# Kernel tuning notes

Measured on AMD Instinct MI355X. Metric: run time of the kernel, lower is better.

Reference implementation:

```python
import jax, jax.numpy as jnp
import numpy as np

N_NODES = 50000
N_EDGES = 800000
F_IN = 256
F_OUT = 64
HEADS = 4
LEAKY_ALPHA = 0.2


def setup_inputs() -> dict:
    key = jax.random.key(0)
    ks = jax.random.split(key, 8)
    x = jax.random.normal(ks[0], (N_NODES, F_IN), dtype=jnp.float32)
    W = jax.random.normal(ks[1], (HEADS, F_IN, F_OUT), dtype=jnp.float32) * 0.05
    a_self = jax.random.normal(ks[2], (HEADS, F_OUT), dtype=jnp.float32) * 0.05
    a_neigh = jax.random.normal(ks[3], (HEADS, F_OUT), dtype=jnp.float32) * 0.05
    bias = jnp.zeros((HEADS, F_OUT), dtype=jnp.float32)
    adj_val = jnp.ones((N_EDGES,), dtype=jnp.float32)
    edge_row = jax.random.randint(ks[4], (N_EDGES,), 0, N_NODES, dtype=jnp.int32)
    edge_col = jax.random.randint(ks[5], (N_EDGES,), 0, N_NODES, dtype=jnp.int32)
    return {"x": x, "W": W, "a_self": a_self, "a_neigh": a_neigh,
            "bias": bias, "adj_val": adj_val,
            "edge_row": edge_row, "edge_col": edge_col}


def reference(x, W, a_self, a_neigh, bias, adj_val, edge_row, edge_col):
    N = x.shape[0]
    # per-head projected features: [H, N, F_out]
    feats = jnp.einsum('nf,hfo->hno', x, W)
    # attention logits per node: [H, N]
    s_self = jnp.einsum('hno,ho->hn', feats, a_self)
    s_neigh = jnp.einsum('hno,ho->hn', feats, a_neigh)
    # edge scores at sparse adjacency positions: [H, E]
    z = s_self[:, edge_row] + s_neigh[:, edge_col]
    e = jnp.where(z > 0, z, LEAKY_ALPHA * z) * adj_val[None, :]

    def seg_softmax(e_h):
        # sparse softmax over each row's nonzero entries
        m = jax.ops.segment_max(e_h, edge_row, num_segments=N)
        ex = jnp.exp(e_h - m[edge_row])
        s = jax.ops.segment_sum(ex, edge_row, num_segments=N)
        return ex / s[edge_row]

    alpha = jax.vmap(seg_softmax)(e)  # [H, E]

    def aggregate(alpha_h, feat_h):
        # sparse-dense matmul: out[i] = sum_{j in N(i)} alpha_ij * feat[j]
        return jax.ops.segment_sum(alpha_h[:, None] * feat_h[edge_col],
                                   edge_row, num_segments=N)

    out = jax.vmap(aggregate)(alpha, feats) + bias[:, None, :]  # [H, N, F_out]
    # concat heads -> [N, H*F_out], then activation
    out = jnp.transpose(out, (1, 0, 2)).reshape(N, -1)
    return jax.nn.relu(out)
```

## Files before the change

### kernel.cpp

```cpp
#include <hip/hip_runtime.h>
#include <hip/hip_fp16.h>
#include <math.h>

#define NN 50000
#define NE 800000
#define FIN 256
#define FOUT 64
#define HEADS 4
#define HF 256
#define CAP 64
#define NBUCK 391
#define BROWS 128
#define CAPB 4096

typedef unsigned short u16;
typedef unsigned int u32;
typedef unsigned long long u64;
typedef __attribute__((ext_vector_type(4))) u16 u16x4;
typedef __attribute__((ext_vector_type(8))) u16 u16x8;
typedef __attribute__((ext_vector_type(8))) short short8;
typedef __attribute__((ext_vector_type(4))) float f32x4;

__device__ __forceinline__ u16 f2bf(float x) {
  u32 u = __float_as_uint(x);
  u += 0x7fffu + ((u >> 16) & 1u);
  return (u16)(u >> 16);
}
__device__ __forceinline__ float bf2f(u16 u) {
  return __uint_as_float(((u32)u) << 16);
}
__device__ __forceinline__ void gload_lds16(u16* lds, const u16* g) {
  __builtin_amdgcn_global_load_lds(
      (const __attribute__((address_space(1))) u32*)g,
      (__attribute__((address_space(3))) u32*)lds, 16, 0, 0);
}

#define BT_B 256
__global__ __launch_bounds__(256) void tiny_pre_k(const float* __restrict__ W,
                                                  u16* __restrict__ Bt,
                                                  int* __restrict__ cntA) {
  const int b = blockIdx.x, tid = threadIdx.x;
  if (b < BT_B) {
    int t = b * 256 + tid;
    int ho = t >> 8, f = t & 255;
    int h = ho >> 6, o = ho & 63;
    Bt[t] = f2bf(W[h * (FIN * FOUT) + f * FOUT + o]);
  } else {
    for (int i = tid; i < NBUCK * 16; i += 256) cntA[i] = 0;
  }
}

__global__ __launch_bounds__(512) void gemm_lg_k(const float* __restrict__ X,
                                                 const u16* __restrict__ Bt,
                                                 u16* __restrict__ C,
                                                 const float* __restrict__ a_self,
                                                 const float* __restrict__ a_neigh,
                                                 float* __restrict__ sself,
                                                 float* __restrict__ sneigh,
                                                 int M) {
  __shared__ __align__(16) u16 smA[128 * 64];
  __shared__ __align__(16) u16 smB[256 * 64];
  const int tid = threadIdx.x;
  const int m0 = blockIdx.x * 128;
  const int lane = tid & 63, wid = tid >> 6;
  const int wr = wid >> 2, wc = wid & 3;
  const int arow = tid >> 3;
  const int acol = (tid & 7) * 8;
  f32x4 acc[4][4] = {};

  for (int k0 = 0; k0 < FIN; k0 += 64) {
    float4 p[2][2];
#pragma unroll
    for (int c = 0; c < 2; ++c) {
      int row = m0 + c * 64 + arow;
      if (row > M - 1) row = M - 1;
      const float* ap = X + (size_t)row * 256 + k0 + acol;
      p[c][0] = *(const float4*)ap;
      p[c][1] = *(const float4*)(ap + 4);
    }
#pragma unroll
    for (int c = 0; c < 4; ++c) {
      int row = c * 64 + arow;
      gload_lds16(&smB[(c * 64 + arow) * 64 + acol], Bt + row * 256 + k0 + acol);
    }
#pragma unroll
    for (int c = 0; c < 2; ++c) {
      u16x8 av = { f2bf(p[c][0].x), f2bf(p[c][0].y), f2bf(p[c][0].z), f2bf(p[c][0].w),
                   f2bf(p[c][1].x), f2bf(p[c][1].y), f2bf(p[c][1].z), f2bf(p[c][1].w) };
      *(u16x8*)&smA[(c * 64 + arow) * 64 + acol] = av;
    }
    asm volatile("s_waitcnt vmcnt(0)" ::: "memory");
    __syncthreads();
#pragma unroll
    for (int kk = 0; kk < 2; ++kk) {
      const int kb = kk * 32 + (lane >> 4) * 8;
      short8 aF[4], bF[4];
#pragma unroll
      for (int mi = 0; mi < 4; ++mi)
        aF[mi] = *(const short8*)&smA[(wr * 64 + mi * 16 + (lane & 15)) * 64 + kb];
#pragma unroll
      for (int ni = 0; ni < 4; ++ni)
        bF[ni] = *(const short8*)&smB[(wc * 64 + ni * 16 + (lane & 15)) * 64 + kb];
#pragma unroll
      for (int mi = 0; mi < 4; ++mi)
#pragma unroll
        for (int ni = 0; ni < 4; ++ni)
          acc[mi][ni] = __builtin_amdgcn_mfma_f32_16x16x32_bf16(aF[mi], bF[ni], acc[mi][ni], 0, 0, 0);
    }
    __syncthreads();
  }
#pragma unroll
  for (int mi = 0; mi < 4; ++mi) {
#pragma unroll
    for (int ni = 0; ni < 4; ++ni) {
      f32x4 a = acc[mi][ni];
      int col = wc * 64 + ni * 16 + (lane & 15);
#pragma unroll
      for (int r = 0; r < 4; ++r) {
        int row = m0 + wr * 64 + mi * 16 + (lane >> 4) * 4 + r;
        if (row < M) C[(size_t)row * 256 + col] = f2bf(a[r]);
      }
    }
  }
  float asv[4], anv[4];
#pragma unroll
  for (int ni = 0; ni < 4; ++ni) {
    int col = wc * 64 + ni * 16 + (lane & 15);
    asv[ni] = a_self[col];
    anv[ni] = a_neigh[col];
  }
#pragma unroll
  for (int mi = 0; mi < 4; ++mi) {
#pragma unroll
    for (int r = 0; r < 4; ++r) {
      float ds = 0.f, dn = 0.f;
#pragma unroll
      for (int ni = 0; ni < 4; ++ni) {
        float v = acc[mi][ni][r];
        ds = fmaf(v, asv[ni], ds);
        dn = fmaf(v, anv[ni], dn);
      }
#pragma unroll
      for (int off = 1; off < 16; off <<= 1) {
        ds += __shfl_xor(ds, off, 64);
        dn += __shfl_xor(dn, off, 64);
      }
      if ((lane & 15) == 0) {
        int row = m0 + wr * 64 + mi * 16 + (lane >> 4) * 4 + r;
        if (row < M) {
          sself[row * 4 + wc] = ds;
          sneigh[row * 4 + wc] = dn;
        }
      }
    }
  }
}

__global__ __launch_bounds__(512) void binA_k(const int* __restrict__ erow,
                                              const int* __restrict__ ecol,
                                              const float* __restrict__ adj,
                                              int* __restrict__ cntA,
                                              u64* __restrict__ coarse) {
  __shared__ int hist[NBUCK];
  __shared__ int gbase[NBUCK];
  const int tid = threadIdx.x;
  for (int i = tid; i < NBUCK; i += 512) hist[i] = 0;
  __syncthreads();
  const int e0 = blockIdx.x * 2048 + tid;
  int bk[4], lr[4], rl[4], ok[4];
  u32 rec[4];
#pragma unroll
  for (int j = 0; j < 4; ++j) {
    int e = e0 + j * 512;
    ok[j] = (e < NE);
    int ee = ok[j] ? e : 0;
    int r = erow[ee];
    int c = ecol[ee];
    float av = adj[ee];
    __half ha = __float2half_rn(av);
    bk[j] = r >> 7;
    rl[j] = r & 127;
    rec[j] = (u32)c | ((u32)(*(u16*)&ha) << 16);
    lr[j] = ok[j] ? atomicAdd(&hist[bk[j]], 1) : 0;
  }
  __syncthreads();
  for (int i = tid; i < NBUCK; i += 512) {
    int h = hist[i];
    gbase[i] = h ? atomicAdd(&cntA[i * 16], h) : 0;
  }
  __syncthreads();
#pragma unroll
  for (int j = 0; j < 4; ++j) {
    if (ok[j]) {
      int pos = gbase[bk[j]] + lr[j];
      if (pos < CAPB) {
        u64 v = ((u64)rl[j] << 32) | (u64)rec[j];
        coarse[(size_t)bk[j] * CAPB + pos] = v;
      }
    }
  }
}

__global__ __launch_bounds__(256) void binB_k(const int* __restrict__ cntA,
                                              const u64* __restrict__ coarse,
                                              int* __restrict__ cnt,
                                              u32* __restrict__ slots) {
  __shared__ int lcnt[BROWS];
  const int b = blockIdx.x, tid = threadIdx.x;
  for (int i = tid; i < BROWS; i += 256) lcnt[i] = 0;
  __syncthreads();
  const int n = min(cntA[b * 16], CAPB);
  const u64* src = coarse + (size_t)b * CAPB;
  for (int i = tid; i < n; i += 256) {
    u64 v = src[i];
    int rl = (int)(v >> 32);
    u32 rec = (u32)v;
    int p = atomicAdd(&lcnt[rl], 1);
    if (p < CAP) slots[((size_t)(b * BROWS + rl)) * CAP + p] = rec;
  }
  __syncthreads();
  for (int i = tid; i < BROWS; i += 256) {
    int row = b * BROWS + i;
    if (row < NN) cnt[row] = min(lcnt[i], CAP);
  }
}

#define NODE_B 3125
__global__ __launch_bounds__(256) void node8_k(const int* __restrict__ cnt,
                                               const u32* __restrict__ slots,
                                               const float4* __restrict__ sself4,
                                               const float4* __restrict__ sneigh4,
                                               const u16* __restrict__ fb,
                                               const float* __restrict__ bias,
                                               float* __restrict__ out) {
  const int tid = threadIdx.x;
  const int l = tid & 31;
  const int hsel = l >> 4;
  const int hw0 = blockIdx.x * 8 + (tid >> 5);
  const float4 b0 = ((const float4*)bias)[l];
  const float4 b1 = ((const float4*)bias)[32 + l];

#pragma unroll
  for (int pass = 0; pass < 2; ++pass) {
    const int i = hw0 + pass * 25000;
    const int deg = cnt[i];
    const int beg = i * CAP;
    const float4 ssv = sself4[i];
    float s0 = 0.f, s1 = 0.f;
    float4 acc0 = { 0.f, 0.f, 0.f, 0.f };
    float4 acc1 = { 0.f, 0.f, 0.f, 0.f };

    for (int base = 0; base < deg; base += 32) {
      const int c32 = min(32, deg - base);
      u32 sv = slots[beg + base + min(l, c32 - 1)];
      int colv = (int)(sv & 0xFFFFu);

      int colq[8];
      u16x4 f0[8], f1[8];
#pragma unroll
      for (int q = 0; q < 8; ++q) colq[q] = __shfl(colv, q, 32);
#pragma unroll
      for (int q = 0; q < 8; ++q) {
        const u16* fp = fb + (size_t)colq[q] * HF + l * 4;
        f0[q] = *(const u16x4*)fp;
        f1[q] = *(const u16x4*)(fp + 128);
      }

      u16 ah = (u16)(sv >> 16);
      float av = __half2float(*(const __half*)&ah);
      float4 nb = sneigh4[colv];
      float z0 = ssv.x + nb.x, z1 = ssv.y + nb.y;
      float z2 = ssv.z + nb.z, z3 = ssv.w + nb.w;
      float w0 = __expf((z0 > 0.f ? z0 : 0.2f * z0) * av);
      float w1 = __expf((z1 > 0.f ? z1 : 0.2f * z1) * av);
      float w2 = __expf((z2 > 0.f ? z2 : 0.2f * z2) * av);
      float w3 = __expf((z3 > 0.f ? z3 : 0.2f * z3) * av);
      if (l >= c32) { w0 = 0.f; w1 = 0.f; w2 = 0.f; w3 = 0.f; }
      __half2 h01 = __floats2half2_rn(w0, w1);
      __half2 h23 = __floats2half2_rn(w2, w3);
      u32 wy = *(u32*)&h01, wz = *(u32*)&h23;

      const int c8 = (c32 + 7) & ~7;
      for (int e = 0; e < c8; e += 8) {
        float wa[8], wb[8];
#pragma unroll
        for (int q = 0; q < 8; ++q) {
          u32 y = (u32)__shfl((int)wy, e + q, 32);
          u32 z = (u32)__shfl((int)wz, e + q, 32);
          float2 fy = __half22float2(*(const __half2*)&y);
          float2 fz = __half22float2(*(const __half2*)&z);
          wa[q] = hsel ? fy.y : fy.x;
          wb[q] = hsel ? fz.y : fz.x;
        }
#pragma unroll
        for (int q = 0; q < 8; ++q) {
          s0 += wa[q];
          s1 += wb[q];
          acc0.x = fmaf(wa[q], bf2f(f0[q][0]), acc0.x);
          acc0.y = fmaf(wa[q], bf2f(f0[q][1]), acc0.y);
          acc0.z = fmaf(wa[q], bf2f(f0[q][2]), acc0.z);
          acc0.w = fmaf(wa[q], bf2f(f0[q][3]), acc0.w);
          acc1.x = fmaf(wb[q], bf2f(f1[q][0]), acc1.x);
          acc1.y = fmaf(wb[q], bf2f(f1[q][1]), acc1.y);
          acc1.z = fmaf(wb[q], bf2f(f1[q][2]), acc1.z);
          acc1.w = fmaf(wb[q], bf2f(f1[q][3]), acc1.w);
        }
        if (e + 8 < c8) {
#pragma unroll
          for (int q = 0; q < 8; ++q) colq[q] = __shfl(colv, e + 8 + q, 32);
#pragma unroll
          for (int q = 0; q < 8; ++q) {
            const u16* fp = fb + (size_t)colq[q] * HF + l * 4;
            f0[q] = *(const u16x4*)fp;
            f1[q] = *(const u16x4*)(fp + 128);
          }
        }
      }
    }
    const float rs0 = (s0 > 0.f) ? __frcp_rn(s0) : 0.f;
    const float rs1 = (s1 > 0.f) ? __frcp_rn(s1) : 0.f;
    float4 o0, o1;
    o0.x = fmaxf(fmaf(acc0.x, rs0, b0.x), 0.f);
    o0.y = fmaxf(fmaf(acc0.y, rs0, b0.y), 0.f);
    o0.z = fmaxf(fmaf(acc0.z, rs0, b0.z), 0.f);
    o0.w = fmaxf(fmaf(acc0.w, rs0, b0.w), 0.f);
    o1.x = fmaxf(fmaf(acc1.x, rs1, b1.x), 0.f);
    o1.y = fmaxf(fmaf(acc1.y, rs1, b1.y), 0.f);
    o1.z = fmaxf(fmaf(acc1.z, rs1, b1.z), 0.f);
    o1.w = fmaxf(fmaf(acc1.w, rs1, b1.w), 0.f);
    ((float4*)out)[(size_t)i * 64 + l] = o0;
    ((float4*)out)[(size_t)i * 64 + 32 + l] = o1;
  }
}

extern "C" void kernel_launch(void* const* d_in, const int* in_sizes, int n_in,
                              void* d_out, int out_size, void* d_ws, size_t ws_size,
                              hipStream_t stream) {
  const float* x       = (const float*)d_in[0];
  const float* W       = (const float*)d_in[1];
  const float* a_self  = (const float*)d_in[2];
  const float* a_neigh = (const float*)d_in[3];
  const float* bias    = (const float*)d_in[4];
  const float* adj     = (const float*)d_in[5];
  const int*   erow    = (const int*)d_in[6];
  const int*   ecol    = (const int*)d_in[7];
  float* out = (float*)d_out;

  char* w = (char*)d_ws;
  u16*   Bt     = (u16*)w;   w += 131072;
  u16*   fb     = (u16*)w;   w += 25600000;
  float* sself  = (float*)w; w += 800000;
  float* sneigh = (float*)w; w += 800000;
  int*   cntA   = (int*)w;   w += NBUCK * 16 * 4;
  int*   cnt    = (int*)w;   w += 200192;
  u32*   slots  = (u32*)w;   w += NN * CAP * 4;
  u64*   coarse = (u64*)w;   w += (size_t)NBUCK * CAPB * 8;

  tiny_pre_k<<<dim3(BT_B + 1), dim3(256), 0, stream>>>(W, Bt, cntA);
  binA_k<<<dim3(NBUCK), dim3(512), 0, stream>>>(erow, ecol, adj, cntA, coarse);
  binB_k<<<dim3(NBUCK), dim3(256), 0, stream>>>(cntA, coarse, cnt, slots);
  gemm_lg_k<<<dim3((NN + 127) / 128), dim3(512), 0, stream>>>(x, Bt, fb, a_self, a_neigh,
                                                              sself, sneigh, NN);
  node8_k<<<dim3(NODE_B), dim3(256), 0, stream>>>(cnt, slots,
                                                  (const float4*)sself,
                                                  (const float4*)sneigh,
                                                  fb, bias, out);
}
```

Baseline: 121.4 us.

## Merge weight conversion into binA and binB into GEMM kernel launches

Folds the W-to-bf16 transpose into extra blocks of the binning kernel and runs the second binning pass as extra blocks of the GEMM kernel. The counter clear moves to a memset. This cuts the kernel launch count and lets the independent binB work overlap with the GEMM. The cost is that binB blocks now carry the GEMM's large LDS footprint and 512-thread shape, which may reduce occupancy. The GEMM grid size (NN+127)/128 equals NBUCK, so the block split is consistent.

```diff
diff --git a/kernel.cpp b/kernel.cpp
--- a/kernel.cpp
+++ b/kernel.cpp
@@ -12,6 +12,7 @@
 #define NBUCK 391
 #define BROWS 128
 #define CAPB 4096
+#define BT_BLOCKS 32
 
 typedef unsigned short u16;
 typedef unsigned int u32;
@@ -35,135 +36,28 @@
       (__attribute__((address_space(3))) u32*)lds, 16, 0, 0);
 }
 
-#define BT_B 256
-__global__ __launch_bounds__(256) void tiny_pre_k(const float* __restrict__ W,
-                                                  u16* __restrict__ Bt,
-                                                  int* __restrict__ cntA) {
-  const int b = blockIdx.x, tid = threadIdx.x;
-  if (b < BT_B) {
-    int t = b * 256 + tid;
-    int ho = t >> 8, f = t & 255;
-    int h = ho >> 6, o = ho & 63;
-    Bt[t] = f2bf(W[h * (FIN * FOUT) + f * FOUT + o]);
-  } else {
-    for (int i = tid; i < NBUCK * 16; i += 256) cntA[i] = 0;
-  }
-}
-
-__global__ __launch_bounds__(512) void gemm_lg_k(const float* __restrict__ X,
-                                                 const u16* __restrict__ Bt,
-                                                 u16* __restrict__ C,
-                                                 const float* __restrict__ a_self,
-                                                 const float* __restrict__ a_neigh,
-                                                 float* __restrict__ sself,
-                                                 float* __restrict__ sneigh,
-                                                 int M) {
-  __shared__ __align__(16) u16 smA[128 * 64];
-  __shared__ __align__(16) u16 smB[256 * 64];
-  const int tid = threadIdx.x;
-  const int m0 = blockIdx.x * 128;
-  const int lane = tid & 63, wid = tid >> 6;
-  const int wr = wid >> 2, wc = wid & 3;
-  const int arow = tid >> 3;
-  const int acol = (tid & 7) * 8;
-  f32x4 acc[4][4] = {};
-
-  for (int k0 = 0; k0 < FIN; k0 += 64) {
-    float4 p[2][2];
-#pragma unroll
-    for (int c = 0; c < 2; ++c) {
-      int row = m0 + c * 64 + arow;
-      if (row > M - 1) row = M - 1;
-      const float* ap = X + (size_t)row * 256 + k0 + acol;
-      p[c][0] = *(const float4*)ap;
-      p[c][1] = *(const float4*)(ap + 4);
-    }
-#pragma unroll
-    for (int c = 0; c < 4; ++c) {
-      int row = c * 64 + arow;
-      gload_lds16(&smB[(c * 64 + arow) * 64 + acol], Bt + row * 256 + k0 + acol);
-    }
-#pragma unroll
-    for (int c = 0; c < 2; ++c) {
-      u16x8 av = { f2bf(p[c][0].x), f2bf(p[c][0].y), f2bf(p[c][0].z), f2bf(p[c][0].w),
-                   f2bf(p[c][1].x), f2bf(p[c][1].y), f2bf(p[c][1].z), f2bf(p[c][1].w) };
-      *(u16x8*)&smA[(c * 64 + arow) * 64 + acol] = av;
-    }
-    asm volatile("s_waitcnt vmcnt(0)" ::: "memory");
-    __syncthreads();
-#pragma unroll
-    for (int kk = 0; kk < 2; ++kk) {
-      const int kb = kk * 32 + (lane >> 4) * 8;
-      short8 aF[4], bF[4];
-#pragma unroll
-      for (int mi = 0; mi < 4; ++mi)
-        aF[mi] = *(const short8*)&smA[(wr * 64 + mi * 16 + (lane & 15)) * 64 + kb];
-#pragma unroll
-      for (int ni = 0; ni < 4; ++ni)
-        bF[ni] = *(const short8*)&smB[(wc * 64 + ni * 16 + (lane & 15)) * 64 + kb];
-#pragma unroll
-      for (int mi = 0; mi < 4; ++mi)
-#pragma unroll
-        for (int ni = 0; ni < 4; ++ni)
-          acc[mi][ni] = __builtin_amdgcn_mfma_f32_16x16x32_bf16(aF[mi], bF[ni], acc[mi][ni], 0, 0, 0);
-    }
-    __syncthreads();
-  }
-#pragma unroll
-  for (int mi = 0; mi < 4; ++mi) {
-#pragma unroll
-    for (int ni = 0; ni < 4; ++ni) {
-      f32x4 a = acc[mi][ni];
-      int col = wc * 64 + ni * 16 + (lane & 15);
-#pragma unroll
-      for (int r = 0; r < 4; ++r) {
-        int row = m0 + wr * 64 + mi * 16 + (lane >> 4) * 4 + r;
-        if (row < M) C[(size_t)row * 256 + col] = f2bf(a[r]);
-      }
-    }
-  }
-  float asv[4], anv[4];
-#pragma unroll
-  for (int ni = 0; ni < 4; ++ni) {
-    int col = wc * 64 + ni * 16 + (lane & 15);
-    asv[ni] = a_self[col];
-    anv[ni] = a_neigh[col];
-  }
-#pragma unroll
-  for (int mi = 0; mi < 4; ++mi) {
-#pragma unroll
-    for (int r = 0; r < 4; ++r) {
-      float ds = 0.f, dn = 0.f;
-#pragma unroll
-      for (int ni = 0; ni < 4; ++ni) {
-        float v = acc[mi][ni][r];
-        ds = fmaf(v, asv[ni], ds);
-        dn = fmaf(v, anv[ni], dn);
-      }
-#pragma unroll
-      for (int off = 1; off < 16; off <<= 1) {
-        ds += __shfl_xor(ds, off, 64);
-        dn += __shfl_xor(dn, off, 64);
-      }
-      if ((lane & 15) == 0) {
-        int row = m0 + wr * 64 + mi * 16 + (lane >> 4) * 4 + r;
-        if (row < M) {
-          sself[row * 4 + wc] = ds;
-          sneigh[row * 4 + wc] = dn;
-        }
-      }
-    }
-  }
-}
-
-__global__ __launch_bounds__(512) void binA_k(const int* __restrict__ erow,
-                                              const int* __restrict__ ecol,
-                                              const float* __restrict__ adj,
-                                              int* __restrict__ cntA,
-                                              u64* __restrict__ coarse) {
+__global__ __launch_bounds__(512) void binA_bt_k(const int* __restrict__ erow,
+                                                 const int* __restrict__ ecol,
+                                                 const float* __restrict__ adj,
+                                                 int* __restrict__ cntA,
+                                                 u64* __restrict__ coarse,
+                                                 const float* __restrict__ W,
+                                                 u16* __restrict__ Bt) {
   __shared__ int hist[NBUCK];
   __shared__ int gbase[NBUCK];
   const int tid = threadIdx.x;
+
+  if (blockIdx.x >= NBUCK) {
+    int t0 = (blockIdx.x - NBUCK) * 2048 + tid * 4;
+    int ho = t0 >> 8, f0 = t0 & 255;
+    int h = ho >> 6, o = ho & 63;
+    const float* wp = W + h * (FIN * FOUT) + o;
+    u16x4 v = { f2bf(wp[(f0 + 0) * FOUT]), f2bf(wp[(f0 + 1) * FOUT]),
+                f2bf(wp[(f0 + 2) * FOUT]), f2bf(wp[(f0 + 3) * FOUT]) };
+    *(u16x4*)&Bt[t0] = v;
+    return;
+  }
+
   for (int i = tid; i < NBUCK; i += 512) hist[i] = 0;
   __syncthreads();
   const int e0 = blockIdx.x * 2048 + tid;
@@ -201,27 +95,136 @@
   }
 }
 
-__global__ __launch_bounds__(256) void binB_k(const int* __restrict__ cntA,
-                                              const u64* __restrict__ coarse,
-                                              int* __restrict__ cnt,
-                                              u32* __restrict__ slots) {
+__global__ __launch_bounds__(512) void gemm_binB_k(const float* __restrict__ X,
+                                                   const u16* __restrict__ Bt,
+                                                   u16* __restrict__ C,
+                                                   const float* __restrict__ a_self,
+                                                   const float* __restrict__ a_neigh,
+                                                   float* __restrict__ sself,
+                                                   float* __restrict__ sneigh,
+                                                   const int* __restrict__ cntA,
+                                                   const u64* __restrict__ coarse,
+                                                   int* __restrict__ cnt,
+                                                   u32* __restrict__ slots,
+                                                   int M) {
+  __shared__ __align__(16) u16 smA[128 * 64];
+  __shared__ __align__(16) u16 smB[256 * 64];
   __shared__ int lcnt[BROWS];
-  const int b = blockIdx.x, tid = threadIdx.x;
-  for (int i = tid; i < BROWS; i += 256) lcnt[i] = 0;
-  __syncthreads();
-  const int n = min(cntA[b * 16], CAPB);
-  const u64* src = coarse + (size_t)b * CAPB;
-  for (int i = tid; i < n; i += 256) {
-    u64 v = src[i];
-    int rl = (int)(v >> 32);
-    u32 rec = (u32)v;
-    int p = atomicAdd(&lcnt[rl], 1);
-    if (p < CAP) slots[((size_t)(b * BROWS + rl)) * CAP + p] = rec;
-  }
-  __syncthreads();
-  for (int i = tid; i < BROWS; i += 256) {
-    int row = b * BROWS + i;
-    if (row < NN) cnt[row] = min(lcnt[i], CAP);
+  const int tid = threadIdx.x;
+
+  if (blockIdx.x >= NBUCK) {
+    const int b = blockIdx.x - NBUCK;
+    for (int i = tid; i < BROWS; i += 512) lcnt[i] = 0;
+    __syncthreads();
+    const int n = min(cntA[b * 16], CAPB);
+    const u64* src = coarse + (size_t)b * CAPB;
+    for (int i = tid; i < n; i += 512) {
+      u64 v = src[i];
+      int rl = (int)(v >> 32);
+      u32 rec = (u32)v;
+      int p = atomicAdd(&lcnt[rl], 1);
+      if (p < CAP) slots[((size_t)(b * BROWS + rl)) * CAP + p] = rec;
+    }
+    __syncthreads();
+    for (int i = tid; i < BROWS; i += 512) {
+      int row = b * BROWS + i;
+      if (row < NN) cnt[row] = min(lcnt[i], CAP);
+    }
+    return;
+  }
+
+  const int m0 = blockIdx.x * 128;
+  const int lane = tid & 63, wid = tid >> 6;
+  const int wr = wid >> 2, wc = wid & 3;
+  const int arow = tid >> 3;
+  const int acol = (tid & 7) * 8;
+  f32x4 acc[4][4] = {};
+
+  for (int k0 = 0; k0 < FIN; k0 += 64) {
+    float4 p[2][2];
+#pragma unroll
+    for (int c = 0; c < 2; ++c) {
+      int row = m0 + c * 64 + arow;
+      if (row > M - 1) row = M - 1;
+      const float* ap = X + (size_t)row * 256 + k0 + acol;
+      p[c][0] = *(const float4*)ap;
+      p[c][1] = *(const float4*)(ap + 4);
+    }
+#pragma unroll
+    for (int c = 0; c < 4; ++c) {
+      int row = c * 64 + arow;
+      gload_lds16(&smB[(c * 64 + arow) * 64 + acol], Bt + row * 256 + k0 + acol);
+    }
+#pragma unroll
+    for (int c = 0; c < 2; ++c) {
+      u16x8 av = { f2bf(p[c][0].x), f2bf(p[c][0].y), f2bf(p[c][0].z), f2bf(p[c][0].w),
+                   f2bf(p[c][1].x), f2bf(p[c][1].y), f2bf(p[c][1].z), f2bf(p[c][1].w) };
+      *(u16x8*)&smA[(c * 64 + arow) * 64 + acol] = av;
+    }
+    asm volatile("s_waitcnt vmcnt(0)" ::: "memory");
+    __syncthreads();
+#pragma unroll
+    for (int kk = 0; kk < 2; ++kk) {
+      const int kb = kk * 32 + (lane >> 4) * 8;
+      short8 aF[4], bF[4];
+#pragma unroll
+      for (int mi = 0; mi < 4; ++mi)
+        aF[mi] = *(const short8*)&smA[(wr * 64 + mi * 16 + (lane & 15)) * 64 + kb];
+#pragma unroll
+      for (int ni = 0; ni < 4; ++ni)
+        bF[ni] = *(const short8*)&smB[(wc * 64 + ni * 16 + (lane & 15)) * 64 + kb];
+#pragma unroll
+      for (int mi = 0; mi < 4; ++mi)
+#pragma unroll
+        for (int ni = 0; ni < 4; ++ni)
+          acc[mi][ni] = __builtin_amdgcn_mfma_f32_16x16x32_bf16(aF[mi], bF[ni], acc[mi][ni], 0, 0, 0);
+    }
+    __syncthreads();
+  }
+#pragma unroll
+  for (int mi = 0; mi < 4; ++mi) {
+#pragma unroll
+    for (int ni = 0; ni < 4; ++ni) {
+      f32x4 a = acc[mi][ni];
+      int col = wc * 64 + ni * 16 + (lane & 15);
+#pragma unroll
+      for (int r = 0; r < 4; ++r) {
+        int row = m0 + wr * 64 + mi * 16 + (lane >> 4) * 4 + r;
+        if (row < M) C[(size_t)row * 256 + col] = f2bf(a[r]);
+      }
+    }
+  }
+  float asv[4], anv[4];
+#pragma unroll
+  for (int ni = 0; ni < 4; ++ni) {
+    int col = wc * 64 + ni * 16 + (lane & 15);
+    asv[ni] = a_self[col];
+    anv[ni] = a_neigh[col];
+  }
+#pragma unroll
+  for (int mi = 0; mi < 4; ++mi) {
+#pragma unroll
+    for (int r = 0; r < 4; ++r) {
+      float ds = 0.f, dn = 0.f;
+#pragma unroll
+      for (int ni = 0; ni < 4; ++ni) {
+        float v = acc[mi][ni][r];
+        ds = fmaf(v, asv[ni], ds);
+        dn = fmaf(v, anv[ni], dn);
+      }
+#pragma unroll
+      for (int off = 1; off < 16; off <<= 1) {
+        ds += __shfl_xor(ds, off, 64);
+        dn += __shfl_xor(dn, off, 64);
+      }
+      if ((lane & 15) == 0) {
+        int row = m0 + wr * 64 + mi * 16 + (lane >> 4) * 4 + r;
+        if (row < M) {
+          sself[row * 4 + wc] = ds;
+          sneigh[row * 4 + wc] = dn;
+        }
+      }
+    }
   }
 }
 
@@ -356,11 +359,11 @@
   u32*   slots  = (u32*)w;   w += NN * CAP * 4;
   u64*   coarse = (u64*)w;   w += (size_t)NBUCK * CAPB * 8;
 
-  tiny_pre_k<<<dim3(BT_B + 1), dim3(256), 0, stream>>>(W, Bt, cntA);
-  binA_k<<<dim3(NBUCK), dim3(512), 0, stream>>>(erow, ecol, adj, cntA, coarse);
-  binB_k<<<dim3(NBUCK), dim3(256), 0, stream>>>(cntA, coarse, cnt, slots);
-  gemm_lg_k<<<dim3((NN + 127) / 128), dim3(512), 0, stream>>>(x, Bt, fb, a_self, a_neigh,
-                                                              sself, sneigh, NN);
+  hipMemsetAsync(cntA, 0, NBUCK * 16 * sizeof(int), stream);
+  binA_bt_k<<<dim3(NBUCK + BT_BLOCKS), dim3(512), 0, stream>>>(erow, ecol, adj,
+                                                               cntA, coarse, W, Bt);
+  gemm_binB_k<<<dim3(NBUCK + NBUCK), dim3(512), 0, stream>>>(
+      x, Bt, fb, a_self, a_neigh, sself, sneigh, cntA, coarse, cnt, slots, NN);
   node8_k<<<dim3(NODE_B), dim3(256), 0, stream>>>(cnt, slots,
                                                   (const float4*)sself,
                                                   (const float4*)sneigh,
```

Measured after the change: 114.4 us (median of 2 runs). -5.8%, faster.
